# Performance work log

Measured on AMD Instinct MI355X. Metric: run time of the kernel, lower is better.

Reference implementation:

```python
import jax, jax.numpy as jnp
import numpy as np

D = 1024
H = 16
HD = D // H
DFF = 4 * D
B, L = 2, 2048
EPS = 1e-5


def setup_inputs() -> dict:
    key = jax.random.key(0)
    ks = jax.random.split(key, 12)
    s = lambda fan_in: 1.0 / np.sqrt(fan_in)
    inp = {
        "x": jax.random.normal(ks[0], (B, L, D), jnp.float32),
        "mask": jnp.ones((1, 1, L, L), jnp.bool_),
        "ln_g": jnp.ones((D,), jnp.float32),
        "ln_b": jnp.zeros((D,), jnp.float32),
        "qkv_w": jax.random.uniform(ks[1], (3 * D, D), jnp.float32, -s(D), s(D)),
        "qkv_b": jax.random.uniform(ks[2], (3 * D,), jnp.float32, -s(D), s(D)),
        "wo_w": jax.random.uniform(ks[3], (D, D), jnp.float32, -s(D), s(D)),
        "wo_b": jax.random.uniform(ks[4], (D,), jnp.float32, -s(D), s(D)),
        "m0_w": jax.random.uniform(ks[5], (DFF, D), jnp.float32, -s(D), s(D)),
        "m0_b": jax.random.uniform(ks[6], (DFF,), jnp.float32, -s(D), s(D)),
        "m1_w": jax.random.uniform(ks[7], (D, DFF), jnp.float32, -s(DFF), s(DFF)),
        "m1_b": jax.random.uniform(ks[8], (D,), jnp.float32, -s(DFF), s(DFF)),
    }
    return inp


def _layer_norm(x, g, b):
    mu = jnp.mean(x, axis=-1, keepdims=True)
    var = jnp.var(x, axis=-1, keepdims=True)
    return (x - mu) * jax.lax.rsqrt(var + EPS) * g + b


def reference(x, mask, ln_g, ln_b, qkv_w, qkv_b, wo_w, wo_b, m0_w, m0_b, m1_w, m1_b):
    b, l, d = x.shape
    # --- pre-norm self-attention ---
    xn = _layer_norm(x, ln_g, ln_b)
    qkv = xn @ qkv_w.T + qkv_b                       # [B, L, 3D]
    qkv = qkv.reshape(b, l, 3, H, HD).transpose(2, 0, 3, 1, 4)  # [3, B, H, L, HD]
    q, k, v = qkv[0], qkv[1], qkv[2]
    scores = jnp.einsum("bhld,bhmd->bhlm", q, k) / np.sqrt(HD)  # [B, H, L, L]
    scores = jnp.where(mask, scores, -1e9)
    attn = jax.nn.softmax(scores, axis=-1)
    ctx = jnp.einsum("bhlm,bhmd->bhld", attn, v)     # [B, H, L, HD]
    ctx = ctx.transpose(0, 2, 1, 3).reshape(b, l, d)
    x = x + ctx @ wo_w.T + wo_b
    # --- GELU MLP (same shared LayerNorm params) ---
    xn = _layer_norm(x, ln_g, ln_b)
    h = jax.nn.gelu(xn @ m0_w.T + m0_b, approximate=False)
    return x + h @ m1_w.T + m1_b
```

## Files before the change

kernel.cpp:

```cpp
#include <hip/hip_runtime.h>
#include <hip/hip_bf16.h>
#include <math.h>

#define BL 4096
#define DM 1024
#define NH 16
#define HD 64
#define DFF 4096
#define SEQ 2048
#define EPS 1e-5f
#define QSCALE 0.18033688011112042f

typedef __bf16 bf16x8 __attribute__((ext_vector_type(8)));
typedef float f32x4 __attribute__((ext_vector_type(4)));
typedef float f32x16 __attribute__((ext_vector_type(16)));

__device__ __forceinline__ unsigned short f2bf(float f) {
    __hip_bfloat16 h = __float2bfloat16(f);
    return *reinterpret_cast<unsigned short*>(&h);
}

__device__ __forceinline__ unsigned int pack2bf(float p0, float p1) {
    unsigned int u0 = __builtin_bit_cast(unsigned int, p0) + 0x8000u;
    unsigned int u1 = __builtin_bit_cast(unsigned int, p1) + 0x8000u;
    return __builtin_amdgcn_perm(u1, u0, 0x07060302);
}

__device__ __forceinline__ void gload_lds16(const void* g, void* l) {
    __builtin_amdgcn_global_load_lds(
        (const __attribute__((address_space(1))) unsigned int*)g,
        (__attribute__((address_space(3))) unsigned int*)l,
        16, 0, 0);
}

__global__ __launch_bounds__(256)
void f2b4_kernel(const float* __restrict__ s0, const float* __restrict__ s1,
                 const float* __restrict__ s2, const float* __restrict__ s3,
                 unsigned short* __restrict__ d0, unsigned short* __restrict__ d1,
                 unsigned short* __restrict__ d2, unsigned short* __restrict__ d3,
                 int n0, int n1, int n2, int n3) {
    int i = blockIdx.x * 256 + threadIdx.x;
    const float* s; unsigned short* d; int j = i;
    if (j < n0) { s = s0; d = d0; }
    else if ((j -= n0) < n1) { s = s1; d = d1; }
    else if ((j -= n1) < n2) { s = s2; d = d2; }
    else if ((j -= n2) < n3) { s = s3; d = d3; }
    else return;
    float4 v = ((const float4*)s)[j];
    ushort4 o = {f2bf(v.x), f2bf(v.y), f2bf(v.z), f2bf(v.w)};
    ((ushort4*)d)[j] = o;
}

__global__ __launch_bounds__(256)
void ln_kernel(const float* __restrict__ x, const float* __restrict__ g,
               const float* __restrict__ b, unsigned short* __restrict__ o) {
    int row = blockIdx.x;
    int tid = threadIdx.x;
    const float* xr = x + (size_t)row * DM;
    float4 v = *(const float4*)(xr + tid * 4);
    float s  = v.x + v.y + v.z + v.w;
    float ss = v.x*v.x + v.y*v.y + v.z*v.z + v.w*v.w;
    #pragma unroll
    for (int off = 32; off > 0; off >>= 1) {
        s  += __shfl_down(s, off);
        ss += __shfl_down(ss, off);
    }
    __shared__ float ps[4], pss[4];
    __shared__ float sh_mu, sh_rs;
    int wid = tid >> 6, lane = tid & 63;
    if (lane == 0) { ps[wid] = s; pss[wid] = ss; }
    __syncthreads();
    if (tid == 0) {
        float S = ps[0] + ps[1] + ps[2] + ps[3];
        float SS = pss[0] + pss[1] + pss[2] + pss[3];
        float mu = S * (1.0f / DM);
        float var = SS * (1.0f / DM) - mu * mu;
        sh_mu = mu;
        sh_rs = 1.0f / sqrtf(var + EPS);
    }
    __syncthreads();
    float mu = sh_mu, rs = sh_rs;
    float4 gv = *(const float4*)(g + tid * 4);
    float4 bv = *(const float4*)(b + tid * 4);
    ushort4 ov;
    ov.x = f2bf((v.x - mu) * rs * gv.x + bv.x);
    ov.y = f2bf((v.y - mu) * rs * gv.y + bv.y);
    ov.z = f2bf((v.z - mu) * rs * gv.z + bv.z);
    ov.w = f2bf((v.w - mu) * rs * gv.w + bv.w);
    *(ushort4*)(o + (size_t)row * DM + tid * 4) = ov;
}

template <int EPI, int TN, int BK, typename OUT_T>
__global__ __launch_bounds__(256)
void gemm_bt_mfma(const unsigned short* __restrict__ A,
                  const unsigned short* __restrict__ B,
                  const float* __restrict__ bias, const float* __restrict__ res,
                  OUT_T* __restrict__ C, int M, int N, int K,
                  unsigned short* __restrict__ vt) {
    constexpr int RPC = 512 / BK;
    constexpr int CA  = 128 / RPC;
    constexpr int CB  = TN / RPC;
    constexpr int FJ  = TN / 32;
    __shared__ unsigned short smem[(128 + TN) * BK];
    unsigned short* As = smem;
    unsigned short* Bs = smem + 128 * BK;
    const int tid = threadIdx.x, lane = tid & 63, wave = tid >> 6;

    const int id   = blockIdx.x;
    const int xcd  = id & 7, slot = id >> 3;
    const int R    = (M / 128) >> 3;
    const int by   = xcd * R + (slot % R);
    const int bx   = slot / R;
    const int m0 = by * 128, n0 = bx * TN;
    const int wm = (wave >> 1) * 64, wn = (wave & 1) * (TN / 2);

    const int srow  = (BK == 64) ? (lane >> 3) : (lane >> 4);
    const int sslot = (BK == 64) ? (lane & 7)  : (lane & 15);
    const int fr = lane & 15;
    const int g  = lane >> 4;

    f32x4 acc[4][FJ] = {};

    for (int kt = 0; kt < K; kt += BK) {
        __syncthreads();
        #pragma unroll
        for (int ci = 0; ci < (CA + CB) / 4; ci++) {
            const int c = ci * 4 + wave;
            const bool isA = (c < CA);
            const int cc = isA ? c : c - CA;
            const int cr = cc * RPC + srow;
            const unsigned short* src = (isA ? A + (size_t)(m0 + cr) * K
                                             : B + (size_t)(n0 + cr) * K)
                                        + kt + ((sslot ^ (cr & 7)) * 8);
            gload_lds16(src, (char*)(isA ? As : Bs) + cc * 1024);
        }
        __syncthreads();

        #pragma unroll
        for (int ko = 0; ko < BK / 32; ko++) {
            const int col = (((ko * 4 + g) ^ (fr & 7)) * 8);
            bf16x8 af[4], bfv[FJ];
            #pragma unroll
            for (int i = 0; i < 4; i++)
                af[i] = *(const bf16x8*)(As + (wm + i * 16 + fr) * BK + col);
            #pragma unroll
            for (int j = 0; j < FJ; j++)
                bfv[j] = *(const bf16x8*)(Bs + (wn + j * 16 + fr) * BK + col);
            #pragma unroll
            for (int i = 0; i < 4; i++)
                #pragma unroll
                for (int j = 0; j < FJ; j++)
                    acc[i][j] = __builtin_amdgcn_mfma_f32_16x16x32_bf16(af[i], bfv[j], acc[i][j], 0, 0, 0);
        }
    }

    const int col  = lane & 15;
    const int rowq = (lane >> 4) * 4;
    float bs[FJ];
    #pragma unroll
    for (int j = 0; j < FJ; j++) bs[j] = bias[n0 + wn + j * 16 + col];

    if (EPI == 3 && n0 >= 2048) {
        __syncthreads();
        #pragma unroll
        for (int i = 0; i < 4; i++) {
            const int l0 = wm + i * 16 + rowq;
            #pragma unroll
            for (int j = 0; j < FJ; j++) {
                const int dcol = wn + j * 16 + col;
                float v0 = acc[i][j][0] + bs[j], v1 = acc[i][j][1] + bs[j];
                float v2 = acc[i][j][2] + bs[j], v3 = acc[i][j][3] + bs[j];
                uint2 pk = {pack2bf(v0, v1), pack2bf(v2, v3)};
                char* p = (char*)smem + dcol * 256 +
                          (((l0 >> 3) ^ (dcol & 7)) * 16) + (l0 & 7) * 2;
                *(uint2*)p = pk;
            }
        }
        __syncthreads();
        const int bb = m0 >> 11, lbase = m0 & 2047;
        #pragma unroll
        for (int k = 0; k < 8; k++) {
            const int oid = tid + k * 256;
            const int dcol = oid >> 4, lc = oid & 15;
            uint4 val = *(const uint4*)((const char*)smem + dcol * 256 +
                                        ((lc ^ (dcol & 7)) * 16));
            const int c = n0 + dcol;
            const int d = c & 63, hh2 = (c >> 6) & 15;
            *(uint4*)(vt + ((size_t)((bb * 16 + hh2) * 64 + d)) * 2048 + lbase + lc * 8) = val;
        }
        return;
    }

    #pragma unroll
    for (int i = 0; i < 4; i++) {
        #pragma unroll
        for (int r = 0; r < 4; r++) {
            const size_t row = (size_t)(m0 + wm + i * 16 + rowq + r);
            #pragma unroll
            for (int j = 0; j < FJ; j++) {
                const int c = n0 + wn + j * 16 + col;
                const size_t off = row * N + c;
                float v = acc[i][j][r] + bs[j];
                if (EPI == 1) v += res[off];
                if (EPI == 2) {
                    float u = v * (0.7978845608028654f + 0.035677408136300125f * v * v);
                    float e = __builtin_amdgcn_exp2f(u * 2.885390081777927f);
                    float th = 1.0f - 2.0f * __builtin_amdgcn_rcpf(e + 1.0f);
                    v = 0.5f * v * (1.0f + th);
                }
                if (EPI == 3) {
                    float vq = (c < 1024) ? v * QSCALE : v;
                    ((unsigned short*)C)[off] = f2bf(vq);
                } else if constexpr (sizeof(OUT_T) == 2) {
                    ((unsigned short*)C)[off] = f2bf(v);
                } else {
                    ((float*)C)[off] = v;
                }
            }
        }
    }
}

__global__ __launch_bounds__(512)
void attn_mfma(const unsigned short* __restrict__ qkv,
               const unsigned short* __restrict__ vt,
               unsigned short* __restrict__ ctx) {
    __shared__ unsigned short smem[2][16384];
    const int bid = blockIdx.x;
    const int xcd = bid & 7, sl = bid >> 3;
    const int qt = sl & 15, pg = sl >> 4;
    const int pair = pg * 8 + xcd;
    const int h = pair & 15, b = pair >> 4;
    const int tid = threadIdx.x, lane = tid & 63, wave = tid >> 6;
    const int grp = wave >> 2, w4 = wave & 3;
    const int hh = lane >> 5, mm = lane & 31;
    const int q0 = b * 2048 + qt * 128 + w4 * 32;

    unsigned short* Ks = smem[grp];
    unsigned short* Vt = smem[grp] + 8192;

    bf16x8 qf[4];
    const unsigned short* qb = qkv + (size_t)(q0 + mm) * 3072 + h * 64 + hh * 8;
    #pragma unroll
    for (int s = 0; s < 4; s++) qf[s] = *(const bf16x8*)(qb + s * 16);

    const int skey = lane >> 3;
    const int sgr  = (lane & 7) ^ (skey & 7);
    const unsigned short* kbase = qkv + ((size_t)(b * 2048) + skey) * 3072 + 1024 + h * 64 + sgr * 8;
    const unsigned short* vbase = vt + ((size_t)((b * 16 + h) * 64) + skey) * 2048 + sgr * 8;

    float l_lane = 0.0f;
    f32x16 o_acc[2] = {};
    const int kt0 = grp * 1024;

    for (int ti = 0; ti < 8; ti++) {
        const int kt = kt0 + ti * 128;
        __syncthreads();
        #pragma unroll
        for (int rep = 0; rep < 4; rep++) {
            int c = rep * 4 + w4;
            gload_lds16(kbase + (size_t)(kt + c * 8) * 3072, (char*)Ks + c * 1024);
        }
        #pragma unroll
        for (int rep = 0; rep < 2; rep++) {
            int c = rep * 4 + w4;
            gload_lds16(vbase + (size_t)(c * 8) * 2048 + kt,      (char*)Vt + c * 1024);
            gload_lds16(vbase + (size_t)(c * 8) * 2048 + kt + 64, (char*)Vt + 8192 + c * 1024);
        }
        __syncthreads();

        #pragma unroll
        for (int sub = 0; sub < 2; sub++) {
            f32x16 sT[2] = {};
            #pragma unroll
            for (int t = 0; t < 2; t++)
                #pragma unroll
                for (int s = 0; s < 4; s++) {
                    bf16x8 kf = *(const bf16x8*)(Ks + (sub * 64 + t * 32 + mm) * 64 + ((s * 2 + hh) ^ (mm & 7)) * 8);
                    sT[t] = __builtin_amdgcn_mfma_f32_32x32x16_bf16(kf, qf[s], sT[t], 0, 0, 0);
                }

            unsigned int pk[2][8];
            #pragma unroll
            for (int t = 0; t < 2; t++)
                #pragma unroll
                for (int e = 0; e < 8; e++) {
                    float p0 = __builtin_amdgcn_exp2f(sT[t][2 * e]);
                    float p1 = __builtin_amdgcn_exp2f(sT[t][2 * e + 1]);
                    l_lane += p0 + p1;
                    pk[t][e] = pack2bf(p0, p1);
                }

            #pragma unroll
            for (int w = 0; w < 4; w++) {
                const int t = w >> 1, eb = (w & 1) * 4;
                unsigned int sx = hh ? pk[t][eb + 0] : pk[t][eb + 2];
                unsigned int sy = hh ? pk[t][eb + 1] : pk[t][eb + 3];
                unsigned int rx = (unsigned int)__shfl_xor((int)sx, 32);
                unsigned int ry = (unsigned int)__shfl_xor((int)sy, 32);
                union { unsigned int u[4]; bf16x8 v; } af;
                af.u[0] = hh ? rx : pk[t][eb + 0];
                af.u[1] = hh ? ry : pk[t][eb + 1];
                af.u[2] = hh ? pk[t][eb + 2] : rx;
                af.u[3] = hh ? pk[t][eb + 3] : ry;
                #pragma unroll
                for (int dt = 0; dt < 2; dt++) {
                    bf16x8 vf = *(const bf16x8*)(Vt + sub * 4096 + (dt * 32 + mm) * 64 + ((w * 2 + hh) ^ (mm & 7)) * 8);
                    o_acc[dt] = __builtin_amdgcn_mfma_f32_32x32x16_bf16(af.v, vf, o_acc[dt], 0, 0, 0);
                }
            }
        }
    }

    float l_red = l_lane + __shfl_xor(l_lane, 32);
    __syncthreads();
    float* ox = (float*)smem;
    float* lx = (float*)((char*)smem + 32768);
    if (grp == 1) {
        float* base = ox + w4 * 2048;
        #pragma unroll
        for (int dt = 0; dt < 2; dt++)
            #pragma unroll
            for (int r = 0; r < 16; r++)
                base[(dt * 16 + r) * 64 + lane] = o_acc[dt][r];
        if (hh == 0) lx[w4 * 32 + mm] = l_red;
    }
    __syncthreads();
    if (grp == 1) return;
    {
        float* base = ox + w4 * 2048;
        #pragma unroll
        for (int dt = 0; dt < 2; dt++)
            #pragma unroll
            for (int r = 0; r < 16; r++)
                o_acc[dt][r] += base[(dt * 16 + r) * 64 + lane];
        l_red += lx[w4 * 32 + mm];
    }

    float inv_own = 1.0f / l_red;
    #pragma unroll
    for (int r = 0; r < 16; r++) {
        const int rowq = (r & 3) + 8 * (r >> 2) + 4 * hh;
        float inv = __shfl(inv_own, rowq);
        size_t base = (size_t)(q0 + rowq) * 1024 + h * 64 + mm;
        ctx[base]      = f2bf(o_acc[0][r] * inv);
        ctx[base + 32] = f2bf(o_acc[1][r] * inv);
    }
}

extern "C" void kernel_launch(void* const* d_in, const int* in_sizes, int n_in,
                              void* d_out, int out_size, void* d_ws, size_t ws_size,
                              hipStream_t stream) {
    const float* x     = (const float*)d_in[0];
    const float* ln_g  = (const float*)d_in[2];
    const float* ln_b  = (const float*)d_in[3];
    const float* qkv_w = (const float*)d_in[4];
    const float* qkv_b = (const float*)d_in[5];
    const float* wo_w  = (const float*)d_in[6];
    const float* wo_b  = (const float*)d_in[7];
    const float* m0_w  = (const float*)d_in[8];
    const float* m0_b  = (const float*)d_in[9];
    const float* m1_w  = (const float*)d_in[10];
    const float* m1_b  = (const float*)d_in[11];
    float* out = (float*)d_out;

    char* ws = (char*)d_ws;
    unsigned short* xn_bf  = (unsigned short*)(ws);
    unsigned short* qkv_bf = (unsigned short*)(ws + (size_t)8  * 1024 * 1024);
    unsigned short* vt_bf  = (unsigned short*)(ws + (size_t)32 * 1024 * 1024);
    unsigned short* ctx_bf = (unsigned short*)(ws + (size_t)40 * 1024 * 1024);
    unsigned short* h_bf   = (unsigned short*)(ws + (size_t)48 * 1024 * 1024);
    unsigned short* qkvw_b = (unsigned short*)(ws + (size_t)80 * 1024 * 1024);
    unsigned short* wow_b  = (unsigned short*)(ws + (size_t)86 * 1024 * 1024);
    unsigned short* m0w_b  = (unsigned short*)(ws + (size_t)88 * 1024 * 1024);
    unsigned short* m1w_b  = (unsigned short*)(ws + (size_t)96 * 1024 * 1024);

    {
        int n0 = 3 * DM * DM / 4, n1 = DM * DM / 4, n2 = DFF * DM / 4, n3 = DM * DFF / 4;
        int tot = n0 + n1 + n2 + n3;
        f2b4_kernel<<<(tot + 255) / 256, 256, 0, stream>>>(
            qkv_w, wo_w, m0_w, m1_w, qkvw_b, wow_b, m0w_b, m1w_b, n0, n1, n2, n3);
    }

    ln_kernel<<<BL, 256, 0, stream>>>(x, ln_g, ln_b, xn_bf);
    gemm_bt_mfma<3, 128, 64, unsigned short><<<(3072 / 128) * (BL / 128), 256, 0, stream>>>(
        xn_bf, qkvw_b, qkv_b, nullptr, qkv_bf, BL, 3072, DM, vt_bf);
    attn_mfma<<<2 * NH * (SEQ / 128), 512, 0, stream>>>(qkv_bf, vt_bf, ctx_bf);
    gemm_bt_mfma<1, 64, 64, float><<<(DM / 64) * (BL / 128), 256, 0, stream>>>(
        ctx_bf, wow_b, wo_b, x, out, BL, DM, DM, nullptr);
    ln_kernel<<<BL, 256, 0, stream>>>(out, ln_g, ln_b, xn_bf);
    gemm_bt_mfma<2, 128, 64, unsigned short><<<(DFF / 128) * (BL / 128), 256, 0, stream>>>(
        xn_bf, m0w_b, m0_b, nullptr, h_bf, BL, DFF, DM, nullptr);
    gemm_bt_mfma<1, 64, 128, float><<<(DM / 64) * (BL / 128), 256, 0, stream>>>(
        h_bf, m1w_b, m1_b, out, out, BL, DM, DFF, nullptr);
}
```

Measured before the change: 341.6 us.

## Add dedicated split-K GEMM for MLP down-projection with in-block reduction

Replaces the generic 64x128-tile GEMM for the final MLP projection (K=4096) with a dedicated kernel. It uses 128x128 output tiles and 512 threads split into two wave groups, each covering half of K. The partial sums are reduced through shared memory before the bias and residual epilogue. The aim is to keep more waves in flight per output tile and to reuse tiles more, on a grid of 256 blocks. In exchange it costs more LDS per block and an extra shared-memory reduction step, and each tile now has half as many blocks.

```diff
diff --git a/kernel.cpp b/kernel.cpp
--- a/kernel.cpp
+++ b/kernel.cpp
@@ -222,6 +222,106 @@
 }
 
 __global__ __launch_bounds__(512)
+void gemm_m1_splitk(const unsigned short* __restrict__ A,
+                    const unsigned short* __restrict__ B,
+                    const float* __restrict__ bias,
+                    const float* __restrict__ res,
+                    float* __restrict__ C) {
+    __shared__ unsigned short smem[2][2][16384];
+    const int id   = blockIdx.x;
+    const int xcd  = id & 7, slot = id >> 3;
+    const int by   = xcd * 4 + (slot & 3);
+    const int bx   = slot >> 2;
+    const int m0 = by * 128, n0 = bx * 128;
+    const int tid = threadIdx.x, lane = tid & 63, wave = tid >> 6;
+    const int grp = wave >> 2, w4 = wave & 3;
+    const int wm = (w4 >> 1) * 64, wn = (w4 & 1) * 64;
+    const int srow = lane >> 3, sslot = lane & 7;
+    const int fr = lane & 15, g = lane >> 4;
+    const int kg0 = grp * 2048;
+
+    f32x4 acc[4][4] = {};
+
+    auto stage = [&](int b, int kt) {
+        unsigned short* As = smem[grp][b];
+        unsigned short* Bs = smem[grp][b] + 8192;
+        #pragma unroll
+        for (int rep = 0; rep < 8; rep++) {
+            const int c = rep * 4 + w4;
+            const bool isA = (c < 16);
+            const int cc = isA ? c : c - 16;
+            const int cr = cc * 8 + srow;
+            const unsigned short* src = (isA ? A + (size_t)(m0 + cr) * 4096
+                                             : B + (size_t)(n0 + cr) * 4096)
+                                        + kt + ((sslot ^ (cr & 7)) * 8);
+            gload_lds16(src, (char*)(isA ? As : Bs) + cc * 1024);
+        }
+    };
+
+    stage(0, kg0);
+    for (int ti = 0; ti < 32; ti++) {
+        __syncthreads();
+        if (ti + 1 < 32) stage((ti + 1) & 1, kg0 + (ti + 1) * 64);
+        const unsigned short* As = smem[grp][ti & 1];
+        const unsigned short* Bs = As + 8192;
+        #pragma unroll
+        for (int ko = 0; ko < 2; ko++) {
+            const int col = (((ko * 4 + g) ^ (fr & 7)) * 8);
+            bf16x8 af[4], bfv[4];
+            #pragma unroll
+            for (int i = 0; i < 4; i++)
+                af[i] = *(const bf16x8*)(As + (wm + i * 16 + fr) * 64 + col);
+            #pragma unroll
+            for (int j = 0; j < 4; j++)
+                bfv[j] = *(const bf16x8*)(Bs + (wn + j * 16 + fr) * 64 + col);
+            #pragma unroll
+            for (int i = 0; i < 4; i++)
+                #pragma unroll
+                for (int j = 0; j < 4; j++)
+                    acc[i][j] = __builtin_amdgcn_mfma_f32_16x16x32_bf16(af[i], bfv[j], acc[i][j], 0, 0, 0);
+        }
+    }
+
+    __syncthreads();
+    float* ox = (float*)smem;
+    if (grp == 1) {
+        float* bp = ox + w4 * 4096;
+        #pragma unroll
+        for (int i = 0; i < 4; i++)
+            #pragma unroll
+            for (int j = 0; j < 4; j++)
+                *(f32x4*)(bp + (i * 4 + j) * 256 + lane * 4) = acc[i][j];
+    }
+    __syncthreads();
+    if (grp == 1) return;
+    {
+        float* bp = ox + w4 * 4096;
+        #pragma unroll
+        for (int i = 0; i < 4; i++)
+            #pragma unroll
+            for (int j = 0; j < 4; j++)
+                acc[i][j] += *(const f32x4*)(bp + (i * 4 + j) * 256 + lane * 4);
+    }
+
+    const int col = lane & 15, rowq = (lane >> 4) * 4;
+    float bs[4];
+    #pragma unroll
+    for (int j = 0; j < 4; j++) bs[j] = bias[n0 + wn + j * 16 + col];
+    #pragma unroll
+    for (int i = 0; i < 4; i++)
+        #pragma unroll
+        for (int r = 0; r < 4; r++) {
+            const size_t row = (size_t)(m0 + wm + i * 16 + rowq + r);
+            #pragma unroll
+            for (int j = 0; j < 4; j++) {
+                const int c = n0 + wn + j * 16 + col;
+                const size_t off = row * 1024 + c;
+                C[off] = acc[i][j][r] + bs[j] + res[off];
+            }
+        }
+}
+
+__global__ __launch_bounds__(512)
 void attn_mfma(const unsigned short* __restrict__ qkv,
                const unsigned short* __restrict__ vt,
                unsigned short* __restrict__ ctx) {
@@ -391,6 +491,5 @@
     ln_kernel<<<BL, 256, 0, stream>>>(out, ln_g, ln_b, xn_bf);
     gemm_bt_mfma<2, 128, 64, unsigned short><<<(DFF / 128) * (BL / 128), 256, 0, stream>>>(
         xn_bf, m0w_b, m0_b, nullptr, h_bf, BL, DFF, DM, nullptr);
-    gemm_bt_mfma<1, 64, 128, float><<<(DM / 64) * (BL / 128), 256, 0, stream>>>(
-        h_bf, m1w_b, m1_b, out, out, BL, DM, DFF, nullptr);
-}
+    gemm_m1_splitk<<<256, 512, 0, stream>>>(h_bf, m1w_b, m1_b, out, out);
+}
```

New measurement: 322.2 us. 5.7% less time.
